# Kernel optimization log

Measured on AMD Instinct MI355X. Metric: run time of the kernel, lower is better.

The kernel has to match this reference:

```python
import jax, jax.numpy as jnp
import numpy as np

NUM_EMBEDDINGS = 512
EMBEDDING_DIM = 256
COMMITMENT_COST = 0.25


def setup_inputs() -> dict:
    key = jax.random.key(0)
    k1, k2 = jax.random.split(key)
    z_e = jax.random.normal(k1, (16, EMBEDDING_DIM, 16, 16, 16), dtype=jnp.float32)
    # codebook init: uniform(-1/K, 1/K) as in the torch module
    codebook = jax.random.uniform(
        k2, (NUM_EMBEDDINGS, EMBEDDING_DIM), dtype=jnp.float32,
        minval=-1.0 / NUM_EMBEDDINGS, maxval=1.0 / NUM_EMBEDDINGS)
    return {"z_e": z_e, "codebook": codebook}


def reference(z_e, codebook):
    # z_e: [B, C, D, H, W] -> [B, D, H, W, C]
    z_p = jnp.transpose(z_e, (0, 2, 3, 4, 1))
    spatial_shape = z_p.shape[:-1]
    flat = z_p.reshape(-1, EMBEDDING_DIM)                      # [N, C]
    z_sq = jnp.sum(flat * flat, axis=1, keepdims=True)         # [N, 1]
    cb_sq = jnp.sum(codebook * codebook, axis=1)[None, :]      # [1, K]
    dot = flat @ codebook.T                                    # [N, K]
    distances = z_sq + cb_sq - 2.0 * dot
    idx = jnp.argmin(distances, axis=1)                        # [N]
    z_q_p = codebook[idx].reshape(z_p.shape)                   # [B, D, H, W, C]
    codebook_loss = jnp.mean((z_q_p - jax.lax.stop_gradient(z_p)) ** 2)
    commitment_loss = jnp.mean((z_p - jax.lax.stop_gradient(z_q_p)) ** 2)
    vq_loss = codebook_loss + COMMITMENT_COST * commitment_loss
    # straight-through estimator
    z_q_st = z_p + jax.lax.stop_gradient(z_q_p - z_p)
    z_q = jnp.transpose(z_q_st, (0, 4, 1, 2, 3))               # [B, C, D, H, W]
    encoding_indices = idx.reshape(spatial_shape)
    return z_q, vq_loss, encoding_indices
```

## Files before the change

kernel.cpp:

```cpp
#include <hip/hip_runtime.h>

#define NPOS   65536
#define CDIM   256
#define KCODES 512
#define ZTOT   16777216
#define IDX_OFF (ZTOT + 1)
#define TAU    2.0e-3f
#define GL_CAP 16384

#define WS_CBSQ 64
#define WS_CBBF 66112
#define WS_GLI  132096
#define NC_FULL 0x7fff

using bf16x8 = __attribute__((ext_vector_type(8))) short;
using f32x4  = __attribute__((ext_vector_type(4))) float;

__device__ __forceinline__ unsigned short f2bf(float f) {
    unsigned int u = __float_as_uint(f);
    return (unsigned short)((u + 0x7fffu + ((u >> 16) & 1u)) >> 16);
}

__device__ __forceinline__ float np_pw128_sq(const float* a) {
    float r[8];
    #pragma unroll
    for (int j = 0; j < 8; ++j) r[j] = __fmul_rn(a[j], a[j]);
    #pragma unroll 1
    for (int i = 8; i < 128; i += 8) {
        #pragma unroll
        for (int j = 0; j < 8; ++j)
            r[j] = __fadd_rn(r[j], __fmul_rn(a[i + j], a[i + j]));
    }
    return __fadd_rn(__fadd_rn(__fadd_rn(r[0], r[1]), __fadd_rn(r[2], r[3])),
                     __fadd_rn(__fadd_rn(r[4], r[5]), __fadd_rn(r[6], r[7])));
}

__global__ void vq_cvtprep(const float* __restrict__ cb, float* __restrict__ ws) {
    const int k = blockIdx.x;
    const int c = threadIdx.x;
    __shared__ float row[256];
    __shared__ float chres[16];
    const float v = cb[(size_t)k * CDIM + c];
    row[c] = v;
    unsigned short* cbf2 = (unsigned short*)(ws + WS_CBBF);
    const int kt = c >> 5, g = (c & 31) >> 3, j = c & 7;
    cbf2[((((k >> 4) * 8 + kt) * 64) + g * 16 + (k & 15)) * 8 + j] = f2bf(v);
    if (k == 0 && c == 0) { ws[0] = 0.0f; ((int*)ws)[1] = 0; }
    __syncthreads();
    if (c < 16) {
        const float* a = &row[(c & 8) * 16];
        const int jj = c & 7;
        float r = __fmul_rn(a[jj], a[jj]);
        #pragma unroll 1
        for (int m = 1; m < 16; ++m)
            r = __fadd_rn(r, __fmul_rn(a[jj + 8 * m], a[jj + 8 * m]));
        chres[c] = r;
    }
    __syncthreads();
    if (c == 0) {
        float h0 = __fadd_rn(__fadd_rn(__fadd_rn(chres[0], chres[1]), __fadd_rn(chres[2], chres[3])),
                             __fadd_rn(__fadd_rn(chres[4], chres[5]), __fadd_rn(chres[6], chres[7])));
        float h1 = __fadd_rn(__fadd_rn(__fadd_rn(chres[8], chres[9]), __fadd_rn(chres[10], chres[11])),
                             __fadd_rn(__fadd_rn(chres[12], chres[13]), __fadd_rn(chres[14], chres[15])));
        ws[WS_CBSQ + k] = __fadd_rn(h0, h1);
    }
}

__device__ __forceinline__ void stw(unsigned short A[2][8][64][8], int nb,
                                    int c, int q, float4 v) {
    const int kt = c >> 5, gg = (c & 31) >> 3, j = c & 7;
    unsigned short* d = &A[nb][kt][gg * 16 + q * 4][j];
    d[0]  = f2bf(v.x);
    d[8]  = f2bf(v.y);
    d[16] = f2bf(v.z);
    d[24] = f2bf(v.w);
}

__launch_bounds__(512, 2)
__global__ void vq_screen(const float* __restrict__ z,
                          float* __restrict__ ws,
                          float* __restrict__ out) {
    const int t  = threadIdx.x;
    const int w  = t >> 6;
    const int l  = t & 63;
    const int g  = l >> 4;
    const int c0 = l & 15;
    int* wsi = (int*)ws;
    const unsigned short* cbf2 = (const unsigned short*)(ws + WS_CBBF);

    __shared__ unsigned short ldsA[2][8][64][8];
    __shared__ float cbsq_s[KCODES];
    __shared__ float red_v[8][16];
    __shared__ int   red_i[8][16];
    __shared__ float fv1[16];
    __shared__ int   ccnt[16];
    __shared__ int   candk[16][8];

    cbsq_s[t] = ws[WS_CBSQ + t];
    if (t < 16) ccnt[t] = 0;

    bf16x8 bfr[4][8];
    #pragma unroll
    for (int p = 0; p < 4; ++p)
        #pragma unroll
        for (int kt = 0; kt < 8; ++kt)
            bfr[p][kt] = *(const bf16x8*)(cbf2 + ((((w * 4 + p) * 8 + kt) * 64 + l) << 3));

    const int base = blockIdx.x * 256;
    const float* zB = z + (size_t)(base >> 12) * 1048576;
    const int c1 = t >> 2, q = t & 3;

    {
        const float* zb = zB + (base & 4095);
        float4 a0 = *(const float4*)(zb + (size_t)c1 * 4096 + q * 4);
        float4 a1 = *(const float4*)(zb + (size_t)(c1 + 128) * 4096 + q * 4);
        stw(ldsA, 0, c1, q, a0);
        stw(ldsA, 0, c1 + 128, q, a1);
    }
    __syncthreads();

    #pragma unroll 1
    for (int it = 0; it < 16; ++it) {
        const int buf = it & 1;
        const int m0  = base + it * 16;

        float4 p0, p1;
        if (it < 15) {
            const float* zb = zB + ((m0 + 16) & 4095);
            p0 = *(const float4*)(zb + (size_t)c1 * 4096 + q * 4);
            p1 = *(const float4*)(zb + (size_t)(c1 + 128) * 4096 + q * 4);
        }

        f32x4 acc[4];
        #pragma unroll
        for (int p = 0; p < 4; ++p) acc[p] = (f32x4){0.f, 0.f, 0.f, 0.f};

        #pragma unroll
        for (int kt = 0; kt < 8; ++kt) {
            const bf16x8 a = *(const bf16x8*)&ldsA[buf][kt][l][0];
            acc[0] = __builtin_amdgcn_mfma_f32_16x16x32_bf16(a, bfr[0][kt], acc[0], 0, 0, 0);
            acc[1] = __builtin_amdgcn_mfma_f32_16x16x32_bf16(a, bfr[1][kt], acc[1], 0, 0, 0);
            acc[2] = __builtin_amdgcn_mfma_f32_16x16x32_bf16(a, bfr[2][kt], acc[2], 0, 0, 0);
            acc[3] = __builtin_amdgcn_mfma_f32_16x16x32_bf16(a, bfr[3][kt], acc[3], 0, 0, 0);
        }

        float v1[4]; int i1[4];
        #pragma unroll
        for (int r = 0; r < 4; ++r) { v1[r] = 3.4028235e38f; i1[r] = 0; }
        #pragma unroll
        for (int p = 0; p < 4; ++p) {
            const int k = w * 64 + p * 16 + c0;
            const float cq = cbsq_s[k];
            #pragma unroll
            for (int r = 0; r < 4; ++r) {
                const float s = fmaf(-2.0f, acc[p][r], cq);
                if (s < v1[r]) { v1[r] = s; i1[r] = k; }
            }
        }
        #pragma unroll
        for (int r = 0; r < 4; ++r) {
            #pragma unroll
            for (int m = 1; m < 16; m <<= 1) {
                float pv = __shfl_xor(v1[r], m, 64);
                int   pi = __shfl_xor(i1[r], m, 64);
                if (pv < v1[r] || (pv == v1[r] && pi < i1[r])) { v1[r] = pv; i1[r] = pi; }
            }
        }
        if (c0 == 0) {
            #pragma unroll
            for (int r = 0; r < 4; ++r) {
                red_v[w][g * 4 + r] = v1[r];
                red_i[w][g * 4 + r] = i1[r];
            }
        }
        __syncthreads();

        if (t < 16) {
            float gv = red_v[0][t]; int gi = red_i[0][t];
            #pragma unroll
            for (int ww = 1; ww < 8; ++ww) {
                const float pv = red_v[ww][t];
                const int   pi = red_i[ww][t];
                if (pv < gv || (pv == gv && pi < gi)) { gv = pv; gi = pi; }
            }
            fv1[t] = gv;
            out[IDX_OFF + m0 + t] = (float)gi;
        }
        __syncthreads();

        #pragma unroll
        for (int p = 0; p < 4; ++p) {
            const int k = w * 64 + p * 16 + c0;
            const float cq = cbsq_s[k];
            #pragma unroll
            for (int r = 0; r < 4; ++r) {
                const float s = fmaf(-2.0f, acc[p][r], cq);
                const int row = g * 4 + r;
                if (s < fv1[row] + TAU) {
                    int pos = atomicAdd(&ccnt[row], 1);
                    if (pos < 8) candk[row][pos] = k;
                }
            }
        }
        if (it < 15) {
            stw(ldsA, buf ^ 1, c1, q, p0);
            stw(ldsA, buf ^ 1, c1 + 128, q, p1);
        }
        __syncthreads();

        if (t < 16) {
            const int nc = ccnt[t];
            if (nc > 1) {
                int slot = atomicAdd(wsi + 1, 1);
                if (slot < GL_CAP) {
                    int* gl = wsi + WS_GLI + slot * 10;
                    gl[0] = m0 + t;
                    gl[1] = (nc > 8) ? NC_FULL : nc;
                    #pragma unroll
                    for (int qq = 0; qq < 8; ++qq)
                        gl[2 + qq] = (qq < nc && qq < 8) ? candk[t][qq] : 0;
                }
            }
            ccnt[t] = 0;
        }
    }
}

__global__ void vq_refine(const float* __restrict__ z,
                          const float* __restrict__ cb,
                          float* __restrict__ ws,
                          float* __restrict__ out) {
    int* wsi = (int*)ws;
    const int cnt = min(wsi[1], GL_CAP);
    const int t   = threadIdx.x;
    const int wid = t >> 6;
    const int l   = t & 63;

    __shared__ __align__(16) float zs[260];
    __shared__ float chres[16];
    __shared__ float zsq_sh;
    __shared__ float wbv[4];
    __shared__ int   wbi[4];

    for (int slot = blockIdx.x; slot < cnt; slot += gridDim.x) {
        __syncthreads();
        const int* gl = wsi + WS_GLI + slot * 10;
        const int n  = gl[0];
        const int nc = gl[1];
        const size_t zb = (size_t)(n >> 12) * 1048576 + (size_t)(n & 4095);
        zs[t] = z[zb + (size_t)t * 4096];
        __syncthreads();

        if (t < 16) {
            const float* a = &zs[(t & 8) * 16];
            const int j = t & 7;
            float r = __fmul_rn(a[j], a[j]);
            #pragma unroll 1
            for (int m = 1; m < 16; ++m)
                r = __fadd_rn(r, __fmul_rn(a[j + 8 * m], a[j + 8 * m]));
            chres[t] = r;
        }
        __syncthreads();
        if (t == 0) {
            float h0 = __fadd_rn(__fadd_rn(__fadd_rn(chres[0], chres[1]), __fadd_rn(chres[2], chres[3])),
                                 __fadd_rn(__fadd_rn(chres[4], chres[5]), __fadd_rn(chres[6], chres[7])));
            float h1 = __fadd_rn(__fadd_rn(__fadd_rn(chres[8], chres[9]), __fadd_rn(chres[10], chres[11])),
                                 __fadd_rn(__fadd_rn(chres[12], chres[13]), __fadd_rn(chres[14], chres[15])));
            zsq_sh = __fadd_rn(h0, h1);
        }
        __syncthreads();
        const float zsq = zsq_sh;
        const float4 zl = *(const float4*)&zs[4 * l];

        float bv = 3.4028235e38f;
        int   bi = 0x7fffffff;
        if (nc != NC_FULL) {
            for (int ci = wid; ci < nc; ci += 4) {
                const int k = gl[2 + ci];
                const float4 e = *(const float4*)(cb + (size_t)k * CDIM + 4 * l);
                double d = (double)e.x * (double)zl.x + (double)e.y * (double)zl.y
                         + (double)e.z * (double)zl.z + (double)e.w * (double)zl.w;
                #pragma unroll
                for (int m = 1; m < 64; m <<= 1)
                    d += __shfl_xor(d, m, 64);
                const float dist = __fsub_rn(__fadd_rn(zsq, ws[WS_CBSQ + k]),
                                             __fmul_rn(2.0f, (float)d));
                if (dist < bv || (dist == bv && k < bi)) { bv = dist; bi = k; }
            }
        } else {
            for (int k = wid; k < KCODES; k += 4) {
                const float4 e = *(const float4*)(cb + (size_t)k * CDIM + 4 * l);
                double d = (double)e.x * (double)zl.x + (double)e.y * (double)zl.y
                         + (double)e.z * (double)zl.z + (double)e.w * (double)zl.w;
                #pragma unroll
                for (int m = 1; m < 64; m <<= 1)
                    d += __shfl_xor(d, m, 64);
                const float dist = __fsub_rn(__fadd_rn(zsq, ws[WS_CBSQ + k]),
                                             __fmul_rn(2.0f, (float)d));
                if (dist < bv || (dist == bv && k < bi)) { bv = dist; bi = k; }
            }
        }
        if (l == 0) { wbv[wid] = bv; wbi[wid] = bi; }
        __syncthreads();
        if (t == 0) {
            float v = wbv[0]; int i = wbi[0];
            #pragma unroll
            for (int ww = 1; ww < 4; ++ww) {
                if (wbv[ww] < v || (wbv[ww] == v && wbi[ww] < i)) { v = wbv[ww]; i = wbi[ww]; }
            }
            out[IDX_OFF + n] = (float)i;
        }
    }
}

__launch_bounds__(512)
__global__ void vq_gather(const float* __restrict__ z,
                          const float* __restrict__ cb,
                          float* __restrict__ out,
                          float* __restrict__ ws) {
    __shared__ int   sidx[64];
    __shared__ float lcb[64][257];
    const int t  = threadIdx.x;
    const int n0 = blockIdx.x * 64;
    const int b  = n0 >> 12;
    const int s0 = n0 & 4095;

    if (t < 64) sidx[t] = (int)out[IDX_OFF + n0 + t];
    __syncthreads();

    {
        const int rlo = t & 7, q4 = t >> 3;
        #pragma unroll
        for (int i = 0; i < 8; ++i) {
            const int r = 8 * i + rlo;
            const float4 v = *(const float4*)(cb + (size_t)sidx[r] * CDIM + q4 * 4);
            lcb[r][q4 * 4 + 0] = v.x;
            lcb[r][q4 * 4 + 1] = v.y;
            lcb[r][q4 * 4 + 2] = v.z;
            lcb[r][q4 * 4 + 3] = v.w;
        }
    }
    __syncthreads();

    float acc = 0.0f;
    const int pq = t & 15, ch0 = t >> 4;
    const size_t zbase = (size_t)b * 1048576 + (size_t)s0;
    #pragma unroll
    for (int pass = 0; pass < 8; ++pass) {
        const int c = pass * 32 + ch0;
        const size_t o = zbase + (size_t)c * 4096 + pq * 4;
        const float4 zv = *(const float4*)(z + o);
        float4 v;
        v.x = lcb[pq * 4 + 0][c];
        v.y = lcb[pq * 4 + 1][c];
        v.z = lcb[pq * 4 + 2][c];
        v.w = lcb[pq * 4 + 3][c];
        *(float4*)(out + o) = v;
        const float dx = v.x - zv.x, dy = v.y - zv.y;
        const float dz = v.z - zv.z, dw = v.w - zv.w;
        acc += dx * dx + dy * dy + dz * dz + dw * dw;
    }

    #pragma unroll
    for (int off = 32; off > 0; off >>= 1)
        acc += __shfl_down(acc, off, 64);
    __shared__ float wsum[8];
    const int lane = t & 63, wid = t >> 6;
    if (lane == 0) wsum[wid] = acc;
    __syncthreads();
    if (t == 0) {
        float bsum = (wsum[0] + wsum[1]) + (wsum[2] + wsum[3])
                   + (wsum[4] + wsum[5]) + (wsum[6] + wsum[7]);
        atomicAdd(&ws[0], bsum);
    }
}

__global__ void vq_fin(const float* __restrict__ ws, float* __restrict__ out) {
    if (threadIdx.x == 0)
        out[ZTOT] = 1.25f * ws[0] / (float)ZTOT;
}

extern "C" void kernel_launch(void* const* d_in, const int* in_sizes, int n_in,
                              void* d_out, int out_size, void* d_ws, size_t ws_size,
                              hipStream_t stream) {
    const float* z  = (const float*)d_in[0];
    const float* cb = (const float*)d_in[1];
    float* out = (float*)d_out;
    float* ws  = (float*)d_ws;

    vq_cvtprep<<<512, 256, 0, stream>>>(cb, ws);
    vq_screen<<<NPOS / 256, 512, 0, stream>>>(z, ws, out);
    vq_refine<<<2048, 256, 0, stream>>>(z, cb, ws, out);
    vq_gather<<<NPOS / 64, 512, 0, stream>>>(z, cb, out, ws);
    vq_fin<<<1, 64, 0, stream>>>(ws, out);
}
```

Before: 156.7 us.

## Compute VQ loss from screening distances instead of rereading z in gather

The loss sum is now built algebraically from ||z||^2, accumulated in the screen kernel from tiles it already loads, plus the winning screened distance (cb_sq - 2 x·e). The refine kernel adds a correction wherever it recomputes a distance. This removes the 64 MB reread of z from the gather kernel, which now only writes the quantized output. The trade-off is that the loss comes from the expanded bf16-screened distance rather than the exact squared difference, which may cost accuracy. The candidate list records are also widened and their capacity doubled.

After: 251.9 us. +60.7%, slower.

```diff
diff --git a/kernel.cpp b/kernel.cpp
--- a/kernel.cpp
+++ b/kernel.cpp
@@ -6,7 +6,7 @@
 #define ZTOT   16777216
 #define IDX_OFF (ZTOT + 1)
 #define TAU    2.0e-3f
-#define GL_CAP 16384
+#define GL_CAP 32768
 
 #define WS_CBSQ 64
 #define WS_CBBF 66112
@@ -95,6 +95,7 @@
     __shared__ float fv1[16];
     __shared__ int   ccnt[16];
     __shared__ int   candk[16][8];
+    __shared__ float wls[8];
 
     cbsq_s[t] = ws[WS_CBSQ + t];
     if (t < 16) ccnt[t] = 0;
@@ -109,6 +110,9 @@
     const int base = blockIdx.x * 256;
     const float* zB = z + (size_t)(base >> 12) * 1048576;
     const int c1 = t >> 2, q = t & 3;
+
+    float lsq = 0.0f;
+    float lsum = 0.0f;
 
     {
         const float* zb = zB + (base & 4095);
@@ -116,6 +120,8 @@
         float4 a1 = *(const float4*)(zb + (size_t)(c1 + 128) * 4096 + q * 4);
         stw(ldsA, 0, c1, q, a0);
         stw(ldsA, 0, c1 + 128, q, a1);
+        lsq += a0.x * a0.x + a0.y * a0.y + a0.z * a0.z + a0.w * a0.w;
+        lsq += a1.x * a1.x + a1.y * a1.y + a1.z * a1.z + a1.w * a1.w;
     }
     __syncthreads();
 
@@ -184,6 +190,7 @@
                 if (pv < gv || (pv == gv && pi < gi)) { gv = pv; gi = pi; }
             }
             fv1[t] = gv;
+            lsum += gv;
             out[IDX_OFF + m0 + t] = (float)gi;
         }
         __syncthreads();
@@ -205,6 +212,8 @@
         if (it < 15) {
             stw(ldsA, buf ^ 1, c1, q, p0);
             stw(ldsA, buf ^ 1, c1 + 128, q, p1);
+            lsq += p0.x * p0.x + p0.y * p0.y + p0.z * p0.z + p0.w * p0.w;
+            lsq += p1.x * p1.x + p1.y * p1.y + p1.z * p1.z + p1.w * p1.w;
         }
         __syncthreads();
 
@@ -213,16 +222,31 @@
             if (nc > 1) {
                 int slot = atomicAdd(wsi + 1, 1);
                 if (slot < GL_CAP) {
-                    int* gl = wsi + WS_GLI + slot * 10;
+                    int* gl = wsi + WS_GLI + slot * 12;
                     gl[0] = m0 + t;
                     gl[1] = (nc > 8) ? NC_FULL : nc;
+                    gl[2] = __float_as_int(fv1[t]);
                     #pragma unroll
                     for (int qq = 0; qq < 8; ++qq)
-                        gl[2 + qq] = (qq < nc && qq < 8) ? candk[t][qq] : 0;
+                        gl[3 + qq] = (qq < nc && qq < 8) ? candk[t][qq] : 0;
                 }
             }
             ccnt[t] = 0;
         }
+    }
+
+    #pragma unroll
+    for (int m = 32; m > 0; m >>= 1)
+        lsq += __shfl_down(lsq, m, 64);
+    if (l == 0) wls[w] = lsq;
+    #pragma unroll
+    for (int m = 1; m < 16; m <<= 1)
+        lsum += __shfl_xor(lsum, m, 64);
+    __syncthreads();
+    if (t == 0) {
+        float tot = ((wls[0] + wls[1]) + (wls[2] + wls[3]))
+                  + ((wls[4] + wls[5]) + (wls[6] + wls[7]));
+        atomicAdd(&ws[0], tot + lsum);
     }
 }
 
@@ -244,9 +268,10 @@
 
     for (int slot = blockIdx.x; slot < cnt; slot += gridDim.x) {
         __syncthreads();
-        const int* gl = wsi + WS_GLI + slot * 10;
+        const int* gl = wsi + WS_GLI + slot * 12;
         const int n  = gl[0];
         const int nc = gl[1];
+        const float dold = __int_as_float(gl[2]);
         const size_t zb = (size_t)(n >> 12) * 1048576 + (size_t)(n & 4095);
         zs[t] = z[zb + (size_t)t * 4096];
         __syncthreads();
@@ -276,7 +301,7 @@
         int   bi = 0x7fffffff;
         if (nc != NC_FULL) {
             for (int ci = wid; ci < nc; ci += 4) {
-                const int k = gl[2 + ci];
+                const int k = gl[3 + ci];
                 const float4 e = *(const float4*)(cb + (size_t)k * CDIM + 4 * l);
                 double d = (double)e.x * (double)zl.x + (double)e.y * (double)zl.y
                          + (double)e.z * (double)zl.z + (double)e.w * (double)zl.w;
@@ -309,15 +334,14 @@
                 if (wbv[ww] < v || (wbv[ww] == v && wbi[ww] < i)) { v = wbv[ww]; i = wbi[ww]; }
             }
             out[IDX_OFF + n] = (float)i;
+            atomicAdd(&ws[0], (v - zsq) - dold);
         }
     }
 }
 
 __launch_bounds__(512)
-__global__ void vq_gather(const float* __restrict__ z,
-                          const float* __restrict__ cb,
-                          float* __restrict__ out,
-                          float* __restrict__ ws) {
+__global__ void vq_gather(const float* __restrict__ cb,
+                          float* __restrict__ out) {
     __shared__ int   sidx[64];
     __shared__ float lcb[64][257];
     const int t  = threadIdx.x;
@@ -342,36 +366,17 @@
     }
     __syncthreads();
 
-    float acc = 0.0f;
     const int pq = t & 15, ch0 = t >> 4;
-    const size_t zbase = (size_t)b * 1048576 + (size_t)s0;
+    const size_t obase = (size_t)b * 1048576 + (size_t)s0;
     #pragma unroll
     for (int pass = 0; pass < 8; ++pass) {
         const int c = pass * 32 + ch0;
-        const size_t o = zbase + (size_t)c * 4096 + pq * 4;
-        const float4 zv = *(const float4*)(z + o);
         float4 v;
         v.x = lcb[pq * 4 + 0][c];
         v.y = lcb[pq * 4 + 1][c];
         v.z = lcb[pq * 4 + 2][c];
         v.w = lcb[pq * 4 + 3][c];
-        *(float4*)(out + o) = v;
-        const float dx = v.x - zv.x, dy = v.y - zv.y;
-        const float dz = v.z - zv.z, dw = v.w - zv.w;
-        acc += dx * dx + dy * dy + dz * dz + dw * dw;
-    }
-
-    #pragma unroll
-    for (int off = 32; off > 0; off >>= 1)
-        acc += __shfl_down(acc, off, 64);
-    __shared__ float wsum[8];
-    const int lane = t & 63, wid = t >> 6;
-    if (lane == 0) wsum[wid] = acc;
-    __syncthreads();
-    if (t == 0) {
-        float bsum = (wsum[0] + wsum[1]) + (wsum[2] + wsum[3])
-                   + (wsum[4] + wsum[5]) + (wsum[6] + wsum[7]);
-        atomicAdd(&ws[0], bsum);
+        *(float4*)(out + obase + (size_t)c * 4096 + pq * 4) = v;
     }
 }
 
@@ -391,6 +396,6 @@
     vq_cvtprep<<<512, 256, 0, stream>>>(cb, ws);
     vq_screen<<<NPOS / 256, 512, 0, stream>>>(z, ws, out);
     vq_refine<<<2048, 256, 0, stream>>>(z, cb, ws, out);
-    vq_gather<<<NPOS / 64, 512, 0, stream>>>(z, cb, out, ws);
+    vq_gather<<<NPOS / 64, 512, 0, stream>>>(cb, out);
     vq_fin<<<1, 64, 0, stream>>>(ws, out);
 }
```
